# Kernel tuning notes

Measured on AMD Instinct MI355X. Metric: run time of the kernel, lower is better.

## Reference

```python
import jax, jax.numpy as jnp
import numpy as np
from jax import lax

E, O, I, K = 8, 256, 128, 3  # num_experts, out_ch, in_ch, kernel
HID = 32  # routing hidden dim


def setup_inputs() -> dict:
    key = jax.random.key(0)
    ks = jax.random.split(key, 7)
    B, H, W = 32, 56, 56
    x = jax.random.normal(ks[0], (B, I, H, W), dtype=jnp.float32)
    # kaiming_normal fan_out for (E,O,I,K,K): fan_out = O*K*K
    std = float(np.sqrt(2.0 / (O * K * K)))
    weight = jax.random.normal(ks[1], (E, O, I, K, K), dtype=jnp.float32) * std
    bias = jax.random.normal(ks[2], (E, O), dtype=jnp.float32)
    # routing MLP: Linear(I,32) -> ReLU -> Linear(32,E) -> softmax
    w1 = jax.random.normal(ks[3], (HID, I), dtype=jnp.float32) / np.sqrt(I)
    b1 = jax.random.normal(ks[4], (HID,), dtype=jnp.float32) * 0.01
    w2 = jax.random.normal(ks[5], (E, HID), dtype=jnp.float32) / np.sqrt(HID)
    b2 = jax.random.normal(ks[6], (E,), dtype=jnp.float32) * 0.01
    return {"x": x, "weight": weight, "bias": bias, "w1": w1, "b1": b1, "w2": w2, "b2": b2}


def reference(x, weight, bias, w1, b1, w2, b2):
    # routing: global avg pool -> MLP -> softmax over experts
    pooled = x.mean(axis=(2, 3))                      # (B, I)
    h = jax.nn.relu(pooled @ w1.T + b1)               # (B, 32)
    r = jax.nn.softmax(h @ w2.T + b2, axis=1)         # (B, E)
    # per-sample combined kernel and bias
    cw = jnp.einsum('be,eoihw->boihw', r, weight)     # (B, O, I, K, K)
    cb = r @ bias                                     # (B, O)
    # per-sample conv (equivalent to groups=batch trick), stride=1, padding=1
    def conv_one(xi, wi):
        return lax.conv_general_dilated(
            xi[None], wi, window_strides=(1, 1), padding=[(1, 1), (1, 1)],
            dimension_numbers=('NCHW', 'OIHW', 'NCHW'))[0]
    out = jax.vmap(conv_one)(x, cw)                   # (B, O, H, W)
    return out + cb[:, :, None, None]
```

## Files before the change

kernel.cpp:

```cpp
#include <hip/hip_runtime.h>

#define E_ 8
#define O_ 256
#define I_ 128
#define B_ 32
#define H_ 56
#define W_ 56
#define HP 58
#define HW (H_*W_)
#define KK 9

#define NROW 4
#define NPIX 224
#define PPIX 348

typedef __attribute__((ext_vector_type(8))) short short8;
typedef __attribute__((ext_vector_type(4))) float float4_;

#define XP_ELEMS (B_*HP*HP*I_)
#define POOL_OFF ((size_t)XP_ELEMS*2)
#define R_OFF    (POOL_OFF + (size_t)B_*H_*I_*4)
#define CWT_OFF  (R_OFF + (size_t)B_*E_*4)

__device__ __forceinline__ unsigned short f2bf(float f) {
  union { float f; unsigned u; } v; v.f = f;
  unsigned r = v.u + 0x7FFFu + ((v.u >> 16) & 1u);
  return (unsigned short)(r >> 16);
}

__device__ __forceinline__ void gload16(const unsigned short* g, unsigned short* l) {
  __builtin_amdgcn_global_load_lds(
      (const __attribute__((address_space(1))) unsigned int*)g,
      (__attribute__((address_space(3))) unsigned int*)l, 16, 0, 0);
}

__global__ void k1_pool_pack(const float* __restrict__ x,
                             unsigned short* __restrict__ xp,
                             float* __restrict__ pooled_part) {
  __shared__ float lds[I_*57];
  const int h = blockIdx.x, b = blockIdx.y, tid = threadIdx.x;
  const float* xb = x + (size_t)b*I_*HW + h*W_;
  for (int idx = tid; idx < I_*14; idx += 256) {
    int ic = idx / 14, w4 = (idx - ic*14)*4;
    float4_ v = *(const float4_*)(xb + (size_t)ic*HW + w4);
    lds[ic*57 + w4 + 0] = v[0];
    lds[ic*57 + w4 + 1] = v[1];
    lds[ic*57 + w4 + 2] = v[2];
    lds[ic*57 + w4 + 3] = v[3];
  }
  __syncthreads();
  if (tid < I_) {
    float s = 0.f;
    #pragma unroll 8
    for (int wv = 0; wv < W_; ++wv) s += lds[tid*57 + wv];
    pooled_part[(size_t)(b*H_ + h)*I_ + tid] = s;
  }
  unsigned short* xrow = xp + ((size_t)(b*HP + h + 1)*HP)*I_;
  for (int idx2 = tid; idx2 < W_*(I_/2); idx2 += 256) {
    int wv = idx2 >> 6, ic2 = idx2 & 63;
    unsigned short u0 = f2bf(lds[(ic2*2)*57 + wv]);
    unsigned short u1 = f2bf(lds[(ic2*2+1)*57 + wv]);
    *(unsigned*)&xrow[(wv+1)*I_ + ic2*2] = (unsigned)u0 | ((unsigned)u1 << 16);
  }
  if (tid < I_) {
    xrow[0*I_ + tid] = 0;
    xrow[57*I_ + tid] = 0;
  }
  if (h == 0) {
    unsigned short* r0 = xp + (size_t)(b*HP)*HP*I_;
    for (int idx = tid; idx < HP*I_; idx += 256) r0[idx] = 0;
  }
  if (h == H_-1) {
    unsigned short* r57 = xp + (size_t)((b*HP + 57)*HP)*I_;
    for (int idx = tid; idx < HP*I_; idx += 256) r57[idx] = 0;
  }
}

__global__ void k2_route(const float* __restrict__ pooled_part,
                         const float* __restrict__ w1, const float* __restrict__ b1,
                         const float* __restrict__ w2, const float* __restrict__ b2,
                         float* __restrict__ r) {
  __shared__ float p[I_];
  __shared__ float hh[32];
  __shared__ float lg[8];
  const int b = blockIdx.x, tid = threadIdx.x;
  if (tid < I_) {
    float s = 0.f;
    for (int h = 0; h < H_; ++h) s += pooled_part[(size_t)(b*H_ + h)*I_ + tid];
    p[tid] = s * (1.f/HW);
  }
  __syncthreads();
  if (tid < 32) {
    float s = b1[tid];
    for (int i = 0; i < I_; ++i) s += p[i]*w1[tid*I_ + i];
    hh[tid] = s > 0.f ? s : 0.f;
  }
  __syncthreads();
  if (tid < 8) {
    float s = b2[tid];
    for (int j = 0; j < 32; ++j) s += hh[j]*w2[tid*32 + j];
    lg[tid] = s;
  }
  __syncthreads();
  if (tid == 0) {
    float m = lg[0];
    for (int e = 1; e < 8; ++e) m = fmaxf(m, lg[e]);
    float ex[8], sum = 0.f;
    for (int e = 0; e < 8; ++e) { ex[e] = expf(lg[e]-m); sum += ex[e]; }
    float inv = 1.f/sum;
    for (int e = 0; e < 8; ++e) r[b*8 + e] = ex[e]*inv;
  }
}

#define WLS 132
__global__ void k3_combine(const float* __restrict__ weight, const float* __restrict__ r,
                           unsigned short* __restrict__ cwT) {
  __shared__ float wl[E_*9*WLS];
  __shared__ float rl[16*E_];
  const int o = blockIdx.x, tid = threadIdx.x;
  const int b0 = blockIdx.y * 16;
  if (tid < 16*E_) rl[tid] = r[b0*E_ + tid];
  for (int e = 0; e < E_; ++e) {
    const float* wg = weight + (size_t)(e*O_ + o)*1152;
    for (int idx = tid; idx < 1152; idx += 256) {
      int ic = idx / 9, t = idx - ic*9;
      wl[(e*9 + t)*WLS + ic] = wg[idx];
    }
  }
  __syncthreads();
  for (int it = 0; it < 18; ++it) {
    int flat = it*256 + tid;
    int bl = flat / 288;
    int slot = flat - bl*288;
    int t = slot >> 5, ic = (slot & 31) * 4;
    float4_ v = {0.f, 0.f, 0.f, 0.f};
    #pragma unroll
    for (int e = 0; e < E_; ++e) {
      float re = rl[bl*E_ + e];
      float4_ w = *(const float4_*)&wl[(e*9 + t)*WLS + ic];
      v[0] += re*w[0]; v[1] += re*w[1]; v[2] += re*w[2]; v[3] += re*w[3];
    }
    unsigned lo = (unsigned)f2bf(v[0]) | ((unsigned)f2bf(v[1]) << 16);
    unsigned hi = (unsigned)f2bf(v[2]) | ((unsigned)f2bf(v[3]) << 16);
    unsigned* dst = (unsigned*)&cwT[((size_t)((b0 + bl)*KK + t)*O_ + o)*I_ + ic];
    dst[0] = lo; dst[1] = hi;
  }
}

__global__ __launch_bounds__(256, 2)
void k4_conv(const unsigned short* __restrict__ xp,
             const unsigned short* __restrict__ cwT,
             const float* __restrict__ r, const float* __restrict__ bias,
             float* __restrict__ out) {
  __shared__ __align__(16) unsigned short patch[PPIX*64];
  __shared__ __align__(16) unsigned short ldsA[2][128*64];
  __shared__ float cbs[128];

  const int tid  = threadIdx.x;
  const int lane = tid & 63;
  const int wave = tid >> 6;
  const int gr0 = blockIdx.x * NROW;
  const int m0  = blockIdx.y * 128;
  const int b   = blockIdx.z;

  if (tid < 128) {
    float s = 0.f;
    #pragma unroll
    for (int e = 0; e < 8; ++e) s += r[b*8 + e]*bias[e*O_ + m0 + tid];
    cbs[tid] = s;
  }

  const int q = lane >> 4, l16 = lane & 15;
  const int lrow = lane >> 3, chunk = (lane & 7) ^ lrow;
  const int wm0 = (wave >> 1) * 64;
  const int wn0 = (wave & 1) * 112;

  int ainv[4];
  #pragma unroll
  for (int j = 0; j < 4; ++j)
    ainv[j] = (wave*32 + j*8 + lrow)*I_ + chunk*8;
  int rowA[4];
  #pragma unroll
  for (int f = 0; f < 4; ++f) rowA[f] = (wm0 + f*16 + l16)*64;
  int xq[2];
  #pragma unroll
  for (int s = 0; s < 2; ++s) xq[s] = ((s*4 + q) ^ (l16 & 7))*8;
  int bg[7];
  #pragma unroll
  for (int g = 0; g < 7; ++g) {
    int p = wn0 + g*16 + l16;
    int rr_ = p / 56;
    bg[g] = rr_*58 + (p - rr_*56);
  }

  float4_ acc[4][7];
  #pragma unroll
  for (int f = 0; f < 4; ++f)
    #pragma unroll
    for (int g = 0; g < 7; ++g) acc[f][g] = (float4_){0.f, 0.f, 0.f, 0.f};

  const unsigned short* xpb = xp + (size_t)((b*HP + gr0)*HP)*I_;

  for (int icc = 0; icc < 2; ++icc) {
    __syncthreads();
    for (int it = 0; it < 11; ++it) {
      int c = it*256 + tid;
      if (c < PPIX*8) {
        int pp = c >> 3, k8 = c & 7;
        gload16(xpb + (size_t)pp*I_ + icc*64 + ((k8 ^ (pp & 7))*8),
                &patch[c*8]);
      }
    }
    {
      const unsigned short* ab = cwT + ((size_t)(b*KK)*O_ + m0)*I_ + icc*64;
      #pragma unroll
      for (int j = 0; j < 4; ++j)
        gload16(ab + ainv[j], &ldsA[0][(wave*32 + j*8)*64]);
    }
    for (int tap = 0; tap < 9; ++tap) {
      __syncthreads();
      if (tap < 8) {
        const unsigned short* ab = cwT + ((size_t)(b*KK + tap + 1)*O_ + m0)*I_ + icc*64;
        #pragma unroll
        for (int j = 0; j < 4; ++j)
          gload16(ab + ainv[j], &ldsA[(tap + 1) & 1][(wave*32 + j*8)*64]);
      }
      const unsigned short* At = ldsA[tap & 1];
      const int kh = tap / 3, kw = tap - kh*3;
      const int toff = kh*58 + kw;
      #pragma unroll
      for (int s = 0; s < 2; ++s) {
        short8 af[4], bfr[7];
        #pragma unroll
        for (int f = 0; f < 4; ++f) af[f] = *(const short8*)&At[rowA[f] + xq[s]];
        #pragma unroll
        for (int g = 0; g < 7; ++g) {
          int pp = bg[g] + toff;
          bfr[g] = *(const short8*)&patch[pp*64 + (((s*4 + q) ^ (pp & 7))*8)];
        }
        __builtin_amdgcn_s_setprio(1);
        #pragma unroll
        for (int f = 0; f < 4; ++f)
          #pragma unroll
          for (int g = 0; g < 7; ++g)
            acc[f][g] = __builtin_amdgcn_mfma_f32_16x16x32_bf16(af[f], bfr[g], acc[f][g], 0, 0, 0);
        __builtin_amdgcn_s_setprio(0);
      }
    }
  }

  const size_t obase = (size_t)(b*O_ + m0)*HW + gr0*W_;
  #pragma unroll
  for (int g = 0; g < 7; ++g) {
    int p = wn0 + g*16 + l16;
    #pragma unroll
    for (int f = 0; f < 4; ++f) {
      #pragma unroll
      for (int v = 0; v < 4; ++v) {
        int ml = wm0 + f*16 + q*4 + v;
        out[obase + (size_t)ml*HW + p] = acc[f][g][v] + cbs[ml];
      }
    }
  }
}

extern "C" void kernel_launch(void* const* d_in, const int* in_sizes, int n_in,
                              void* d_out, int out_size, void* d_ws, size_t ws_size,
                              hipStream_t stream) {
  const float* x      = (const float*)d_in[0];
  const float* weight = (const float*)d_in[1];
  const float* bias   = (const float*)d_in[2];
  const float* w1     = (const float*)d_in[3];
  const float* b1     = (const float*)d_in[4];
  const float* w2     = (const float*)d_in[5];
  const float* b2     = (const float*)d_in[6];
  float* out = (float*)d_out;
  char* ws = (char*)d_ws;

  unsigned short* xp     = (unsigned short*)(ws);
  float*          ppart  = (float*)(ws + POOL_OFF);
  float*          rr     = (float*)(ws + R_OFF);
  unsigned short* cwT    = (unsigned short*)(ws + CWT_OFF);

  k1_pool_pack<<<dim3(H_, B_), 256, 0, stream>>>(x, xp, ppart);
  k2_route<<<B_, 128, 0, stream>>>(ppart, w1, b1, w2, b2, rr);
  k3_combine<<<dim3(O_, 2), 256, 0, stream>>>(weight, rr, cwT);
  k4_conv<<<dim3(H_/NROW, 2, B_), 256, 0, stream>>>(xp, cwT, rr, bias, out);
}
```

Measured before the change: 249.9 us.

## Fuse routing MLP into combine kernel and pool via atomics

Removes the separate routing kernel. Pooling partial sums are now accumulated with atomicAdd into a zeroed buffer, and each combine block redundantly computes the routing MLP and softmax for all 32 samples before combining weights. The combine grid drops from 512 to 256 blocks, each handling all batches. This saves a launch and the serial per-sample routing kernel, at the cost of 256-fold redundant MLP work, a memset, atomic contention, and fewer, longer combine blocks.

```diff
diff --git a/kernel.cpp b/kernel.cpp
--- a/kernel.cpp
+++ b/kernel.cpp
@@ -9,6 +9,8 @@
 #define HP 58
 #define HW (H_*W_)
 #define KK 9
+#define OI (O_*I_)
+#define HID 32
 
 #define NROW 4
 #define NPIX 224
@@ -36,7 +38,7 @@
 
 __global__ void k1_pool_pack(const float* __restrict__ x,
                              unsigned short* __restrict__ xp,
-                             float* __restrict__ pooled_part) {
+                             float* __restrict__ pooled) {
   __shared__ float lds[I_*57];
   const int h = blockIdx.x, b = blockIdx.y, tid = threadIdx.x;
   const float* xb = x + (size_t)b*I_*HW + h*W_;
@@ -53,7 +55,7 @@
     float s = 0.f;
     #pragma unroll 8
     for (int wv = 0; wv < W_; ++wv) s += lds[tid*57 + wv];
-    pooled_part[(size_t)(b*H_ + h)*I_ + tid] = s;
+    atomicAdd(&pooled[b*I_ + tid], s);
   }
   unsigned short* xrow = xp + ((size_t)(b*HP + h + 1)*HP)*I_;
   for (int idx2 = tid; idx2 < W_*(I_/2); idx2 += 256) {
@@ -76,50 +78,19 @@
   }
 }
 
-__global__ void k2_route(const float* __restrict__ pooled_part,
-                         const float* __restrict__ w1, const float* __restrict__ b1,
-                         const float* __restrict__ w2, const float* __restrict__ b2,
-                         float* __restrict__ r) {
-  __shared__ float p[I_];
-  __shared__ float hh[32];
-  __shared__ float lg[8];
-  const int b = blockIdx.x, tid = threadIdx.x;
-  if (tid < I_) {
-    float s = 0.f;
-    for (int h = 0; h < H_; ++h) s += pooled_part[(size_t)(b*H_ + h)*I_ + tid];
-    p[tid] = s * (1.f/HW);
-  }
-  __syncthreads();
-  if (tid < 32) {
-    float s = b1[tid];
-    for (int i = 0; i < I_; ++i) s += p[i]*w1[tid*I_ + i];
-    hh[tid] = s > 0.f ? s : 0.f;
-  }
-  __syncthreads();
-  if (tid < 8) {
-    float s = b2[tid];
-    for (int j = 0; j < 32; ++j) s += hh[j]*w2[tid*32 + j];
-    lg[tid] = s;
-  }
-  __syncthreads();
-  if (tid == 0) {
-    float m = lg[0];
-    for (int e = 1; e < 8; ++e) m = fmaxf(m, lg[e]);
-    float ex[8], sum = 0.f;
-    for (int e = 0; e < 8; ++e) { ex[e] = expf(lg[e]-m); sum += ex[e]; }
-    float inv = 1.f/sum;
-    for (int e = 0; e < 8; ++e) r[b*8 + e] = ex[e]*inv;
-  }
-}
-
 #define WLS 132
-__global__ void k3_combine(const float* __restrict__ weight, const float* __restrict__ r,
-                           unsigned short* __restrict__ cwT) {
+__global__ void k3_combine(const float* __restrict__ weight,
+                           const float* __restrict__ pooled,
+                           const float* __restrict__ w1, const float* __restrict__ b1,
+                           const float* __restrict__ w2, const float* __restrict__ b2,
+                           unsigned short* __restrict__ cwT, float* __restrict__ rr) {
   __shared__ float wl[E_*9*WLS];
-  __shared__ float rl[16*E_];
+  __shared__ float pl[B_][I_+1];
+  __shared__ float hb[B_][HID+1];
+  __shared__ float lgf[B_][9];
+  __shared__ float rl[B_*E_];
   const int o = blockIdx.x, tid = threadIdx.x;
-  const int b0 = blockIdx.y * 16;
-  if (tid < 16*E_) rl[tid] = r[b0*E_ + tid];
+
   for (int e = 0; e < E_; ++e) {
     const float* wg = weight + (size_t)(e*O_ + o)*1152;
     for (int idx = tid; idx < 1152; idx += 256) {
@@ -127,8 +98,48 @@
       wl[(e*9 + t)*WLS + ic] = wg[idx];
     }
   }
-  __syncthreads();
-  for (int it = 0; it < 18; ++it) {
+  for (int i = tid; i < B_*I_; i += 256)
+    pl[i >> 7][i & 127] = pooled[i] * (1.f/HW);
+  __syncthreads();
+
+  {
+    const int b = tid >> 3, j = tid & 7;
+    float hacc[4];
+    #pragma unroll
+    for (int u = 0; u < 4; ++u) hacc[u] = b1[j*4 + u];
+    for (int i = 0; i < I_; ++i) {
+      float p = pl[b][i];
+      #pragma unroll
+      for (int u = 0; u < 4; ++u) hacc[u] += p * w1[(j*4 + u)*I_ + i];
+    }
+    #pragma unroll
+    for (int u = 0; u < 4; ++u) hb[b][j*4 + u] = hacc[u] > 0.f ? hacc[u] : 0.f;
+  }
+  __syncthreads();
+  {
+    const int b = tid >> 3, e = tid & 7;
+    float s = b2[e];
+    #pragma unroll
+    for (int j = 0; j < HID; ++j) s += hb[b][j] * w2[e*HID + j];
+    lgf[b][e] = s;
+  }
+  __syncthreads();
+  if ((tid & 7) == 0) {
+    const int b = tid >> 3;
+    float m = lgf[b][0];
+    #pragma unroll
+    for (int e = 1; e < E_; ++e) m = fmaxf(m, lgf[b][e]);
+    float ex[E_], sum = 0.f;
+    #pragma unroll
+    for (int e = 0; e < E_; ++e) { ex[e] = expf(lgf[b][e] - m); sum += ex[e]; }
+    float inv = 1.f/sum;
+    #pragma unroll
+    for (int e = 0; e < E_; ++e) rl[b*E_ + e] = ex[e]*inv;
+  }
+  __syncthreads();
+  if (o == 0) rr[tid] = rl[tid];
+
+  for (int it = 0; it < 36; ++it) {
     int flat = it*256 + tid;
     int bl = flat / 288;
     int slot = flat - bl*288;
@@ -142,7 +153,7 @@
     }
     unsigned lo = (unsigned)f2bf(v[0]) | ((unsigned)f2bf(v[1]) << 16);
     unsigned hi = (unsigned)f2bf(v[2]) | ((unsigned)f2bf(v[3]) << 16);
-    unsigned* dst = (unsigned*)&cwT[((size_t)((b0 + bl)*KK + t)*O_ + o)*I_ + ic];
+    unsigned* dst = (unsigned*)&cwT[((size_t)(bl*KK + t)*O_ + o)*I_ + ic];
     dst[0] = lo; dst[1] = hi;
   }
 }
@@ -278,12 +289,12 @@
   char* ws = (char*)d_ws;
 
   unsigned short* xp     = (unsigned short*)(ws);
-  float*          ppart  = (float*)(ws + POOL_OFF);
+  float*          pooled = (float*)(ws + POOL_OFF);
   float*          rr     = (float*)(ws + R_OFF);
   unsigned short* cwT    = (unsigned short*)(ws + CWT_OFF);
 
-  k1_pool_pack<<<dim3(H_, B_), 256, 0, stream>>>(x, xp, ppart);
-  k2_route<<<B_, 128, 0, stream>>>(ppart, w1, b1, w2, b2, rr);
-  k3_combine<<<dim3(O_, 2), 256, 0, stream>>>(weight, rr, cwT);
+  hipMemsetAsync(pooled, 0, (size_t)B_*I_*sizeof(float), stream);
+  k1_pool_pack<<<dim3(H_, B_), 256, 0, stream>>>(x, xp, pooled);
+  k3_combine<<<O_, 256, 0, stream>>>(weight, pooled, w1, b1, w2, b2, cwT, rr);
   k4_conv<<<dim3(H_/NROW, 2, B_), 256, 0, stream>>>(xp, cwT, rr, bias, out);
 }
```

After: 262.1 us. 1.05x slower.
